# Optimization experiments

Measured on AMD Instinct MI355X. Metric: run time of the kernel, lower is better.

The kernel has to match this reference:

```python
import math
import jax, jax.numpy as jnp
import numpy as np

B = 65536
EMBED = 256
COND = 256
TIME = 128
HID = 256
E = 8
RHID = 128
IN_DIM = EMBED + TIME + COND  # 640


def setup_inputs() -> dict:
    key = jax.random.key(0)
    ks = jax.random.split(key, 20)
    s = 0.02
    inp = {
        "z_t": jax.random.normal(ks[0], (B, EMBED), jnp.float32),
        "t": jax.random.uniform(ks[1], (B, 1), jnp.float32),
        "cond": jax.random.normal(ks[2], (B, COND), jnp.float32),
        # time embedding proj (Linear(time,time) -> SiLU -> Linear(time,time))
        "tW1": jax.random.normal(ks[3], (TIME, TIME), jnp.float32) * s,
        "tb1": jnp.zeros((TIME,), jnp.float32),
        "tW2": jax.random.normal(ks[4], (TIME, TIME), jnp.float32) * s,
        "tb2": jnp.zeros((TIME,), jnp.float32),
        # stacked expert weights [E, in, out]
        "eW1": jax.random.normal(ks[5], (E, IN_DIM, HID), jnp.float32) * s,
        "eb1": jnp.zeros((E, HID), jnp.float32),
        "eW2": jax.random.normal(ks[6], (E, HID, HID), jnp.float32) * s,
        "eb2": jnp.zeros((E, HID), jnp.float32),
        "eW3": jax.random.normal(ks[7], (E, HID, EMBED), jnp.float32) * s,
        "eb3": jnp.zeros((E, EMBED), jnp.float32),
        # router
        "rW1": jax.random.normal(ks[8], (IN_DIM, RHID), jnp.float32) * s,
        "rb1": jnp.zeros((RHID,), jnp.float32),
        "rW2": jax.random.normal(ks[9], (RHID, E), jnp.float32) * s,
        "rb2": jnp.zeros((E,), jnp.float32),
    }
    return inp


def _time_embedding(t, tW1, tb1, tW2, tb2):
    half = TIME // 2  # 64
    scale = -math.log(10000.0) / (half - 1)
    freqs = jnp.exp(jnp.arange(half, dtype=t.dtype) * scale)[None, :]  # [1, half]
    angles = t * freqs  # [B, half]
    emb = jnp.concatenate([jnp.sin(angles), jnp.cos(angles)], axis=-1)  # [B, TIME]
    h = jax.nn.silu(emb @ tW1 + tb1)
    return h @ tW2 + tb2


def reference(z_t, t, cond, tW1, tb1, tW2, tb2, eW1, eb1, eW2, eb2, eW3, eb3, rW1, rb1, rW2, rb2):
    time_emb = _time_embedding(t, tW1, tb1, tW2, tb2)
    x = jnp.concatenate([z_t, time_emb, cond], axis=-1)  # [B, IN_DIM]
    # dense MoE: all experts via batched GEMMs (dropout=0 -> identity)
    h1 = jax.nn.silu(jnp.einsum('bi,eih->beh', x, eW1) + eb1)      # [B,E,HID]
    h2 = jax.nn.silu(jnp.einsum('beh,ehk->bek', h1, eW2) + eb2)    # [B,E,HID]
    expert_out = jnp.einsum('beh,ehd->bed', h2, eW3) + eb3         # [B,E,EMBED]
    # router softmax gate
    rh = jax.nn.silu(x @ rW1 + rb1)
    gate = jax.nn.softmax(rh @ rW2 + rb2, axis=-1)                 # [B,E]
    velocity = jnp.einsum('be,bed->bd', gate, expert_out)          # [B,EMBED]
    return velocity, gate
```

## Files before the change

### kernel.cpp

```cpp
#include <hip/hip_runtime.h>

typedef __attribute__((ext_vector_type(8))) short bf16x8;
typedef __attribute__((ext_vector_type(4))) float f32x4;

#define NB_ROWS 65536
#define D_EMBED 256
#define D_HID   256
#define N_EXP   8
#define D_RHID  128
#define D_IN    640
#define D_H1    2048

#define HSTR 264

static __device__ __forceinline__ ushort f2bf(float f) {
  union { float f; unsigned u; } v; v.f = f;
  unsigned r = v.u + 0x7fffu + ((v.u >> 16) & 1u);
  return (ushort)(r >> 16);
}
static __device__ __forceinline__ float bf2f(ushort h) {
  union { unsigned u; float f; } v; v.u = ((unsigned)h) << 16;
  return v.f;
}
static __device__ __forceinline__ float silu_f(float x) {
  return x / (1.0f + __expf(-x));
}

static __device__ __forceinline__ int kswz(int r, int c) {
  return r * 64 + ((((c) >> 3) ^ (r & 7)) << 3) + ((c) & 7);
}
static __device__ __forceinline__ int gswz(int r, int c) {
  return ((c) & ~63) | (((((c) >> 3) & 7) ^ ((r) & 7)) << 3) | ((c) & 7);
}

__global__ void prep_transpose(const float* __restrict__ src, ushort* __restrict__ dst,
                               int R, int C, int total) {
  int idx = blockIdx.x * 256 + threadIdx.x;
  if (idx >= total) return;
  int rc = R * C;
  int m = idx / rc;
  int rem = idx - m * rc;
  int r = rem / C;
  int c = rem - r * C;
  dst[m * rc + c * R + r] = f2bf(src[idx]);
}
__global__ void prep_transpose_swz(const float* __restrict__ src, ushort* __restrict__ dst,
                                   int R, int C, int total) {
  int idx = blockIdx.x * 256 + threadIdx.x;
  if (idx >= total) return;
  int rc = R * C;
  int m = idx / rc;
  int rem = idx - m * rc;
  int r = rem / C;
  int c = rem - r * C;
  int p = (r & ~63) + (((((r >> 3) & 7) ^ (c & 7)) << 3) | (r & 7));
  dst[m * rc + c * R + p] = f2bf(src[idx]);
}

static __device__ __forceinline__ void glA128_512(const ushort* __restrict__ src, int ld,
                                                  int kt, ushort* dst, int tid, int w) {
  #pragma unroll
  for (int c = 0; c < 2; ++c) {
    int f = c * 8192 + tid * 16;
    int r = f >> 7, ce = (f & 127) >> 1;
    __builtin_amdgcn_global_load_lds(
        (const __attribute__((address_space(1))) void*)(src + (size_t)r * ld + kt + ce),
        (__attribute__((address_space(3))) void*)(dst + ((c * 8192 + w * 1024) >> 1)),
        16, 0, 0);
  }
}
static __device__ __forceinline__ void glB256_512(const ushort* __restrict__ src, int ld,
                                                  int kt, ushort* dst, int tid, int w) {
  #pragma unroll
  for (int c = 0; c < 4; ++c) {
    int f = c * 8192 + tid * 16;
    int r = f >> 7, ce = (f & 127) >> 1;
    __builtin_amdgcn_global_load_lds(
        (const __attribute__((address_space(1))) void*)(src + (size_t)r * ld + kt + ce),
        (__attribute__((address_space(3))) void*)(dst + ((c * 8192 + w * 1024) >> 1)),
        16, 0, 0);
  }
}
static __device__ __forceinline__ void glB128_256(const ushort* __restrict__ src, int ld,
                                                  int kt, ushort* dst, int tid, int w) {
  #pragma unroll
  for (int c = 0; c < 4; ++c) {
    int f = c * 4096 + tid * 16;
    int r = f >> 7, ce = (f & 127) >> 1;
    __builtin_amdgcn_global_load_lds(
        (const __attribute__((address_space(1))) void*)(src + (size_t)r * ld + kt + ce),
        (__attribute__((address_space(3))) void*)(dst + ((c * 4096 + w * 1024) >> 1)),
        16, 0, 0);
  }
}

__global__ __launch_bounds__(512) void time_x_kernel(
    const float* __restrict__ zt, const float* __restrict__ tin,
    const float* __restrict__ cond,
    const ushort* __restrict__ tw1t, const ushort* __restrict__ tw2t,
    const float* __restrict__ tb1, const float* __restrict__ tb2,
    ushort* __restrict__ x) {
  __shared__ __align__(16) ushort sE[128 * 136];
  __shared__ float sFreq[64];
  __shared__ float sB1[128];
  __shared__ float sB2[128];

  const int tid = threadIdx.x;
  const int row0 = blockIdx.x * 128;

  for (int ch = tid; ch < 128 * 64; ch += 512) {
    int r = ch >> 6;
    int c4 = (ch & 63) << 2;
    size_t grow = (size_t)(row0 + r);
    float4 zv = *(const float4*)&zt[grow * 256 + c4];
    ushort4 o; o.x = f2bf(zv.x); o.y = f2bf(zv.y); o.z = f2bf(zv.z); o.w = f2bf(zv.w);
    *(ushort4*)&x[grow * 640 + gswz(r, c4)] = o;
    float4 cv = *(const float4*)&cond[grow * 256 + c4];
    ushort4 o2; o2.x = f2bf(cv.x); o2.y = f2bf(cv.y); o2.z = f2bf(cv.z); o2.w = f2bf(cv.w);
    *(ushort4*)&x[grow * 640 + gswz(r, 384 + c4)] = o2;
  }

  if (tid < 64) sFreq[tid] = __expf((float)tid * (-9.210340371976184f / 63.0f));
  if (tid < 128) { sB1[tid] = tb1[tid]; sB2[tid] = tb2[tid]; }
  __syncthreads();

  {
    int r = tid >> 2;
    int qd = tid & 3;
    float tv = tin[row0 + r];
    int half = qd >> 1;
    int cbase = (qd & 1) * 32;
    ushort* er = &sE[r * 136 + half * 64 + cbase];
    #pragma unroll
    for (int c = 0; c < 32; ++c) {
      float a = tv * sFreq[cbase + c];
      float v = half ? __cosf(a) : __sinf(a);
      er[c] = f2bf(v);
    }
  }
  __syncthreads();

  const int l = tid & 63;
  const int w = tid >> 6;
  const int wm = w >> 1;
  const int wn = w & 1;
  const int lr = l & 15;
  const int lk = (l >> 4) * 8;
  const int q4 = (l >> 4) * 4;

  f32x4 acc[2][4] = {};
  #pragma unroll
  for (int kk = 0; kk < 4; ++kk) {
    int kb = kk * 32 + lk;
    bf16x8 av[2], bv[4];
    #pragma unroll
    for (int mf = 0; mf < 2; ++mf)
      av[mf] = *(const bf16x8*)&sE[(wm * 32 + mf * 16 + lr) * 136 + kb];
    #pragma unroll
    for (int nf = 0; nf < 4; ++nf)
      bv[nf] = *(const bf16x8*)&tw1t[(size_t)(wn * 64 + nf * 16 + lr) * 128 + kb];
    #pragma unroll
    for (int mf = 0; mf < 2; ++mf)
      #pragma unroll
      for (int nf = 0; nf < 4; ++nf)
        acc[mf][nf] = __builtin_amdgcn_mfma_f32_16x16x32_bf16(av[mf], bv[nf], acc[mf][nf], 0, 0, 0);
  }
  __syncthreads();
  #pragma unroll
  for (int mf = 0; mf < 2; ++mf)
    #pragma unroll
    for (int nf = 0; nf < 4; ++nf) {
      int cc = wn * 64 + nf * 16 + lr;
      #pragma unroll
      for (int rg = 0; rg < 4; ++rg) {
        int rr = wm * 32 + mf * 16 + q4 + rg;
        sE[rr * 136 + cc] = f2bf(silu_f(acc[mf][nf][rg] + sB1[cc]));
      }
    }
  __syncthreads();

  f32x4 acc2[2][4] = {};
  #pragma unroll
  for (int kk = 0; kk < 4; ++kk) {
    int kb = kk * 32 + lk;
    bf16x8 av[2], bv[4];
    #pragma unroll
    for (int mf = 0; mf < 2; ++mf)
      av[mf] = *(const bf16x8*)&sE[(wm * 32 + mf * 16 + lr) * 136 + kb];
    #pragma unroll
    for (int nf = 0; nf < 4; ++nf)
      bv[nf] = *(const bf16x8*)&tw2t[(size_t)(wn * 64 + nf * 16 + lr) * 128 + kb];
    #pragma unroll
    for (int mf = 0; mf < 2; ++mf)
      #pragma unroll
      for (int nf = 0; nf < 4; ++nf)
        acc2[mf][nf] = __builtin_amdgcn_mfma_f32_16x16x32_bf16(av[mf], bv[nf], acc2[mf][nf], 0, 0, 0);
  }
  #pragma unroll
  for (int mf = 0; mf < 2; ++mf)
    #pragma unroll
    for (int nf = 0; nf < 4; ++nf) {
      int cc = wn * 64 + nf * 16 + lr;
      #pragma unroll
      for (int rg = 0; rg < 4; ++rg) {
        int rr = wm * 32 + mf * 16 + q4 + rg;
        x[(size_t)(row0 + rr) * 640 + gswz(rr, 256 + cc)] = f2bf(acc2[mf][nf][rg] + sB2[cc]);
      }
    }
}

__global__ __launch_bounds__(256) void router_kernel(
    const ushort* __restrict__ xb, const ushort* __restrict__ rw1t,
    const float* __restrict__ rb1, const float* __restrict__ rW2,
    const float* __restrict__ rb2, float* __restrict__ gatef,
    float* __restrict__ gateo) {
  __shared__ __align__(16) ushort smA[128 * 64];
  __shared__ __align__(16) ushort smB[128 * 64];
  __shared__ __align__(16) ushort rhbuf[128 * 136];
  __shared__ float sW2[128 * 8];

  const int tid = threadIdx.x;
  const int row0 = blockIdx.x * 128;
  for (int i = tid; i < 1024; i += 256) sW2[i] = rW2[i];

  const int l = tid & 63;
  const int w = tid >> 6;
  const int wm = w >> 1, wn = w & 1;
  const int lr = l & 15, lk = (l >> 4) * 8, q4 = (l >> 4) * 4;
  const ushort* xrow = xb + (size_t)row0 * 640;

  f32x4 acc[4][4] = {};
  for (int kt = 0; kt < 640; kt += 64) {
    glB128_256(xrow, 640, kt, smA, tid, w);
    glB128_256(rw1t, 640, kt, smB, tid, w);
    __syncthreads();
    #pragma unroll
    for (int kk = 0; kk < 2; ++kk) {
      int kb = kk * 32 + lk;
      bf16x8 av[4], bv[4];
      #pragma unroll
      for (int mf = 0; mf < 4; ++mf)
        av[mf] = *(const bf16x8*)&smA[kswz(wm * 64 + mf * 16 + lr, kb)];
      #pragma unroll
      for (int nf = 0; nf < 4; ++nf)
        bv[nf] = *(const bf16x8*)&smB[kswz(wn * 64 + nf * 16 + lr, kb)];
      #pragma unroll
      for (int mf = 0; mf < 4; ++mf)
        #pragma unroll
        for (int nf = 0; nf < 4; ++nf)
          acc[mf][nf] = __builtin_amdgcn_mfma_f32_16x16x32_bf16(av[mf], bv[nf], acc[mf][nf], 0, 0, 0);
    }
    __syncthreads();
  }
  #pragma unroll
  for (int nf = 0; nf < 4; ++nf) {
    int cc = wn * 64 + nf * 16 + lr;
    float b1v = rb1[cc];
    #pragma unroll
    for (int mf = 0; mf < 4; ++mf)
      #pragma unroll
      for (int rg = 0; rg < 4; ++rg) {
        int rr = wm * 64 + mf * 16 + q4 + rg;
        rhbuf[rr * 136 + cc] = f2bf(silu_f(acc[mf][nf][rg] + b1v));
      }
  }
  __syncthreads();

  if (tid < 128) {
    float a[8];
    #pragma unroll
    for (int e = 0; e < 8; ++e) a[e] = rb2[e];
    #pragma unroll
    for (int i8 = 0; i8 < 16; ++i8) {
      bf16x8 hv = *(const bf16x8*)&rhbuf[tid * 136 + i8 * 8];
      #pragma unroll
      for (int j = 0; j < 8; ++j) {
        float h = bf2f((ushort)hv[j]);
        const float* wrow = &sW2[(i8 * 8 + j) * 8];
        #pragma unroll
        for (int e = 0; e < 8; ++e) a[e] += h * wrow[e];
      }
    }
    float mx = a[0];
    #pragma unroll
    for (int e = 1; e < 8; ++e) mx = fmaxf(mx, a[e]);
    float s = 0.f, ex[8];
    #pragma unroll
    for (int e = 0; e < 8; ++e) { ex[e] = __expf(a[e] - mx); s += ex[e]; }
    float inv = 1.f / s;
    size_t b = (size_t)(row0 + tid);
    #pragma unroll
    for (int e = 0; e < 8; ++e) {
      float g = ex[e] * inv;
      gatef[b * 8 + e] = g;
      gateo[b * 8 + e] = g;
    }
  }
}

__global__ __launch_bounds__(512) void moe_h1_kernel(
    const ushort* __restrict__ xb, const ushort* __restrict__ w1t,
    const float* __restrict__ eb1, ushort* __restrict__ hg, int row_base) {
  __shared__ __align__(16) ushort smA[128 * 64];
  __shared__ __align__(16) ushort smB[256 * 64];

  const int tid = threadIdx.x;
  int nwg = gridDim.x;
  int flat = blockIdx.x;
  int sid = (flat & 7) * (nwg >> 3) + (flat >> 3);
  const int rb = sid >> 3;
  const int e  = sid & 7;
  const int lrow0 = rb * 128;

  const int l = tid & 63;
  const int w = tid >> 6;
  const int wm = w >> 2, wn = w & 3;
  const int lr = l & 15, lk = (l >> 4) * 8, q4 = (l >> 4) * 4;

  const ushort* xrow = xb + (size_t)(row_base + lrow0) * 640;
  const ushort* W1 = w1t + (size_t)e * (256 * 640);

  f32x4 acc[4][4] = {};
  for (int kt = 0; kt < 640; kt += 64) {
    glA128_512(xrow, 640, kt, smA, tid, w);
    glB256_512(W1, 640, kt, smB, tid, w);
    __syncthreads();
    #pragma unroll
    for (int kk = 0; kk < 2; ++kk) {
      int kb = kk * 32 + lk;
      bf16x8 av[4], bv[4];
      #pragma unroll
      for (int mf = 0; mf < 4; ++mf)
        av[mf] = *(const bf16x8*)&smA[kswz(wm * 64 + mf * 16 + lr, kb)];
      #pragma unroll
      for (int nf = 0; nf < 4; ++nf)
        bv[nf] = *(const bf16x8*)&smB[kswz(wn * 64 + nf * 16 + lr, kb)];
      #pragma unroll
      for (int mf = 0; mf < 4; ++mf)
        #pragma unroll
        for (int nf = 0; nf < 4; ++nf)
          acc[mf][nf] = __builtin_amdgcn_mfma_f32_16x16x32_bf16(av[mf], bv[nf], acc[mf][nf], 0, 0, 0);
    }
    __syncthreads();
  }
  #pragma unroll
  for (int nf = 0; nf < 4; ++nf) {
    int cc = wn * 64 + nf * 16 + lr;
    float b1v = eb1[e * 256 + cc];
    #pragma unroll
    for (int mf = 0; mf < 4; ++mf)
      #pragma unroll
      for (int rg = 0; rg < 4; ++rg) {
        int rr = wm * 64 + mf * 16 + q4 + rg;
        hg[(size_t)(lrow0 + rr) * D_H1 + e * 256 + gswz(rr, cc)] =
            f2bf(silu_f(acc[mf][nf][rg] + b1v));
      }
  }
}

__global__ __launch_bounds__(512) void moe_h2_kernel(
    ushort* __restrict__ hg, const ushort* __restrict__ w2t,
    const float* __restrict__ eb2, const float* __restrict__ gatef, int row_base) {
  __shared__ __align__(16) ushort smA[128 * 64];
  __shared__ __align__(16) ushort smB[256 * 64];
  __shared__ float sGate[128];

  const int tid = threadIdx.x;
  int nwg = gridDim.x;
  int flat = blockIdx.x;
  int sid = (flat & 7) * (nwg >> 3) + (flat >> 3);
  const int rb = sid >> 3;
  const int e  = sid & 7;
  const int lrow0 = rb * 128;

  const int l = tid & 63;
  const int w = tid >> 6;
  const int wm = w >> 2, wn = w & 3;
  const int lr = l & 15, lk = (l >> 4) * 8, q4 = (l >> 4) * 4;

  if (tid < 128) sGate[tid] = gatef[(size_t)(row_base + lrow0 + tid) * 8 + e];

  ushort* hrow = hg + (size_t)lrow0 * D_H1 + e * 256;
  const ushort* W2 = w2t + (size_t)e * (256 * 256);

  f32x4 acc[4][4] = {};
  for (int kt = 0; kt < 256; kt += 64) {
    glA128_512(hrow, D_H1, kt, smA, tid, w);
    glB256_512(W2, 256, kt, smB, tid, w);
    __syncthreads();
    #pragma unroll
    for (int kk = 0; kk < 2; ++kk) {
      int kb = kk * 32 + lk;
      bf16x8 av[4], bv[4];
      #pragma unroll
      for (int mf = 0; mf < 4; ++mf)
        av[mf] = *(const bf16x8*)&smA[kswz(wm * 64 + mf * 16 + lr, kb)];
      #pragma unroll
      for (int nf = 0; nf < 4; ++nf)
        bv[nf] = *(const bf16x8*)&smB[kswz(wn * 64 + nf * 16 + lr, kb)];
      #pragma unroll
      for (int mf = 0; mf < 4; ++mf)
        #pragma unroll
        for (int nf = 0; nf < 4; ++nf)
          acc[mf][nf] = __builtin_amdgcn_mfma_f32_16x16x32_bf16(av[mf], bv[nf], acc[mf][nf], 0, 0, 0);
    }
    __syncthreads();
  }
  #pragma unroll
  for (int nf = 0; nf < 4; ++nf) {
    int cc = wn * 64 + nf * 16 + lr;
    float b2v = eb2[e * 256 + cc];
    #pragma unroll
    for (int mf = 0; mf < 4; ++mf)
      #pragma unroll
      for (int rg = 0; rg < 4; ++rg) {
        int rr = wm * 64 + mf * 16 + q4 + rg;
        hrow[(size_t)rr * D_H1 + gswz(rr, cc)] =
            f2bf(silu_f(acc[mf][nf][rg] + b2v) * sGate[rr]);
      }
  }
}

__global__ __launch_bounds__(512) void moe_vel_kernel(
    const ushort* __restrict__ hg, const ushort* __restrict__ w3t,
    const float* __restrict__ eb3, const float* __restrict__ gatef,
    float* __restrict__ velout, int row_base) {
  __shared__ __align__(16) ushort smA[128 * 64];
  __shared__ __align__(16) ushort smB[256 * 64];
  __shared__ float sGate[128 * 8];

  const int tid = threadIdx.x;
  int nwg = gridDim.x;
  int flat = blockIdx.x;
  int sid = (flat & 7) * (nwg >> 3) + (flat >> 3);
  const int lrow0 = sid * 128;

  const int l = tid & 63;
  const int w = tid >> 6;
  const int wm = w >> 2, wn = w & 3;
  const int lr = l & 15, lk = (l >> 4) * 8, q4 = (l >> 4) * 4;

  for (int i = tid; i < 1024; i += 512) sGate[i] = gatef[(size_t)(row_base + lrow0) * 8 + i];

  const ushort* hrow = hg + (size_t)lrow0 * D_H1;
  f32x4 vacc[4][4] = {};
  __syncthreads();

  for (int kt = 0; kt < 2048; kt += 64) {
    const int e = kt >> 8;
    glA128_512(hrow, D_H1, kt, smA, tid, w);
    glB256_512(w3t + (size_t)e * (256 * 256), 256, kt & 255, smB, tid, w);
    __syncthreads();
    #pragma unroll
    for (int kk = 0; kk < 2; ++kk) {
      int kb = kk * 32 + lk;
      bf16x8 av[4], bv[4];
      #pragma unroll
      for (int mf = 0; mf < 4; ++mf)
        av[mf] = *(const bf16x8*)&smA[kswz(wm * 64 + mf * 16 + lr, kb)];
      #pragma unroll
      for (int nf = 0; nf < 4; ++nf)
        bv[nf] = *(const bf16x8*)&smB[kswz(wn * 64 + nf * 16 + lr, kb)];
      #pragma unroll
      for (int mf = 0; mf < 4; ++mf)
        #pragma unroll
        for (int nf = 0; nf < 4; ++nf)
          vacc[mf][nf] = __builtin_amdgcn_mfma_f32_16x16x32_bf16(av[mf], bv[nf], vacc[mf][nf], 0, 0, 0);
    }
    __syncthreads();
  }

  float* eL = (float*)smB;
  for (int i = tid; i < 2048; i += 512) eL[i] = eb3[i];
  __syncthreads();
  #pragma unroll
  for (int mf = 0; mf < 4; ++mf)
    #pragma unroll
    for (int rg = 0; rg < 4; ++rg) {
      int rr = wm * 64 + mf * 16 + q4 + rg;
      const float* gp = &sGate[rr * 8];
      #pragma unroll
      for (int nf = 0; nf < 4; ++nf) {
        int cc = wn * 64 + nf * 16 + lr;
        float bsum = 0.f;
        #pragma unroll
        for (int ee = 0; ee < 8; ++ee) bsum += gp[ee] * eL[ee * 256 + cc];
        velout[(size_t)(row_base + lrow0 + rr) * D_EMBED + cc] = vacc[mf][nf][rg] + bsum;
      }
    }
}

__global__ __launch_bounds__(512) void moe_fused_kernel(
    const ushort* __restrict__ xb, const ushort* __restrict__ w1t,
    const ushort* __restrict__ w2t, const ushort* __restrict__ w3t,
    const float* __restrict__ eb1, const float* __restrict__ eb2,
    const float* __restrict__ eb3, const float* __restrict__ gatef,
    float* __restrict__ velout) {
  __shared__ __align__(16) ushort smA[128 * 64];
  __shared__ __align__(16) ushort smB[256 * 64];
  __shared__ __align__(16) ushort hbuf[128 * HSTR];
  __shared__ float sGate[128 * 8];
  __shared__ float sEb3[8 * 256];

  const int tid = threadIdx.x;
  const int row0 = blockIdx.x * 128;
  const int l = tid & 63;
  const int w = tid >> 6;
  const int wm = w >> 2, wn = w & 3;
  const int lr = l & 15, lk = (l >> 4) * 8, q4 = (l >> 4) * 4;

  for (int i = tid; i < 1024; i += 512) sGate[i] = gatef[(size_t)row0 * 8 + i];
  for (int i = tid; i < 2048; i += 512) sEb3[i] = eb3[i];

  const ushort* xrow = xb + (size_t)row0 * 640;
  f32x4 vacc[4][4] = {};
  __syncthreads();

  for (int e = 0; e < 8; ++e) {
    const ushort* W1 = w1t + (size_t)e * (256 * 640);
    const ushort* W2 = w2t + (size_t)e * (256 * 256);
    const ushort* W3 = w3t + (size_t)e * (256 * 256);

    f32x4 acc[4][4] = {};
    for (int kt = 0; kt < 640; kt += 64) {
      glA128_512(xrow, 640, kt, smA, tid, w);
      glB256_512(W1, 640, kt, smB, tid, w);
      __syncthreads();
      #pragma unroll
      for (int kk = 0; kk < 2; ++kk) {
        int kb = kk * 32 + lk;
        bf16x8 av[4], bv[4];
        #pragma unroll
        for (int mf = 0; mf < 4; ++mf)
          av[mf] = *(const bf16x8*)&smA[kswz(wm * 64 + mf * 16 + lr, kb)];
        #pragma unroll
        for (int nf = 0; nf < 4; ++nf)
          bv[nf] = *(const bf16x8*)&smB[kswz(wn * 64 + nf * 16 + lr, kb)];
        #pragma unroll
        for (int mf = 0; mf < 4; ++mf)
          #pragma unroll
          for (int nf = 0; nf < 4; ++nf)
            acc[mf][nf] = __builtin_amdgcn_mfma_f32_16x16x32_bf16(av[mf], bv[nf], acc[mf][nf], 0, 0, 0);
      }
      __syncthreads();
    }
    #pragma unroll
    for (int nf = 0; nf < 4; ++nf) {
      int cc = wn * 64 + nf * 16 + lr;
      float b1v = eb1[e * 256 + cc];
      #pragma unroll
      for (int mf = 0; mf < 4; ++mf)
        #pragma unroll
        for (int rg = 0; rg < 4; ++rg) {
          int rr = wm * 64 + mf * 16 + q4 + rg;
          hbuf[rr * HSTR + cc] = f2bf(silu_f(acc[mf][nf][rg] + b1v));
        }
    }
    __syncthreads();

    #pragma unroll
    for (int mf = 0; mf < 4; ++mf)
      #pragma unroll
      for (int nf = 0; nf < 4; ++nf)
        acc[mf][nf] = (f32x4){0.f, 0.f, 0.f, 0.f};
    for (int kt = 0; kt < 256; kt += 64) {
      glB256_512(W2, 256, kt, smB, tid, w);
      __syncthreads();
      #pragma unroll
      for (int kk = 0; kk < 2; ++kk) {
        int kbl = kk * 32 + lk;
        int kbh = kt + kbl;
        bf16x8 av[4], bv[4];
        #pragma unroll
        for (int mf = 0; mf < 4; ++mf)
          av[mf] = *(const bf16x8*)&hbuf[(wm * 64 + mf * 16 + lr) * HSTR + kbh];
        #pragma unroll
        for (int nf = 0; nf < 4; ++nf)
          bv[nf] = *(const bf16x8*)&smB[kswz(wn * 64 + nf * 16 + lr, kbl)];
        #pragma unroll
        for (int mf = 0; mf < 4; ++mf)
          #pragma unroll
          for (int nf = 0; nf < 4; ++nf)
            acc[mf][nf] = __builtin_amdgcn_mfma_f32_16x16x32_bf16(av[mf], bv[nf], acc[mf][nf], 0, 0, 0);
      }
      __syncthreads();
    }
    #pragma unroll
    for (int nf = 0; nf < 4; ++nf) {
      int cc = wn * 64 + nf * 16 + lr;
      float b2v = eb2[e * 256 + cc];
      #pragma unroll
      for (int mf = 0; mf < 4; ++mf)
        #pragma unroll
        for (int rg = 0; rg < 4; ++rg) {
          int rr = wm * 64 + mf * 16 + q4 + rg;
          float gv = sGate[rr * 8 + e];
          hbuf[rr * HSTR + cc] = f2bf(silu_f(acc[mf][nf][rg] + b2v) * gv);
        }
    }
    __syncthreads();

    for (int kt = 0; kt < 256; kt += 64) {
      glB256_512(W3, 256, kt, smB, tid, w);
      __syncthreads();
      #pragma unroll
      for (int kk = 0; kk < 2; ++kk) {
        int kbl = kk * 32 + lk;
        int kbh = kt + kbl;
        bf16x8 av[4], bv[4];
        #pragma unroll
        for (int mf = 0; mf < 4; ++mf)
          av[mf] = *(const bf16x8*)&hbuf[(wm * 64 + mf * 16 + lr) * HSTR + kbh];
        #pragma unroll
        for (int nf = 0; nf < 4; ++nf)
          bv[nf] = *(const bf16x8*)&smB[kswz(wn * 64 + nf * 16 + lr, kbl)];
        #pragma unroll
        for (int mf = 0; mf < 4; ++mf)
          #pragma unroll
          for (int nf = 0; nf < 4; ++nf)
            vacc[mf][nf] = __builtin_amdgcn_mfma_f32_16x16x32_bf16(av[mf], bv[nf], vacc[mf][nf], 0, 0, 0);
      }
      __syncthreads();
    }
  }

  #pragma unroll
  for (int mf = 0; mf < 4; ++mf)
    #pragma unroll
    for (int rg = 0; rg < 4; ++rg) {
      int rr = wm * 64 + mf * 16 + q4 + rg;
      const float* gp = &sGate[rr * 8];
      #pragma unroll
      for (int nf = 0; nf < 4; ++nf) {
        int cc = wn * 64 + nf * 16 + lr;
        float bsum = 0.f;
        #pragma unroll
        for (int ee = 0; ee < 8; ++ee) bsum += gp[ee] * sEb3[ee * 256 + cc];
        velout[(size_t)(row0 + rr) * D_EMBED + cc] = vacc[mf][nf][rg] + bsum;
      }
    }
}

extern "C" void kernel_launch(void* const* d_in, const int* in_sizes, int n_in,
                              void* d_out, int out_size, void* d_ws, size_t ws_size,
                              hipStream_t stream) {
  const float* zt   = (const float*)d_in[0];
  const float* tin  = (const float*)d_in[1];
  const float* cond = (const float*)d_in[2];
  const float* tW1  = (const float*)d_in[3];
  const float* tb1  = (const float*)d_in[4];
  const float* tW2  = (const float*)d_in[5];
  const float* tb2  = (const float*)d_in[6];
  const float* eW1  = (const float*)d_in[7];
  const float* eb1  = (const float*)d_in[8];
  const float* eW2  = (const float*)d_in[9];
  const float* eb2  = (const float*)d_in[10];
  const float* eW3  = (const float*)d_in[11];
  const float* eb3  = (const float*)d_in[12];
  const float* rW1  = (const float*)d_in[13];
  const float* rb1  = (const float*)d_in[14];
  const float* rW2  = (const float*)d_in[15];
  const float* rb2  = (const float*)d_in[16];

  char* wp = (char*)d_ws;
  ushort* xb    = (ushort*)wp; wp += (size_t)NB_ROWS * D_IN * 2;
  float*  gatef = (float*)wp;  wp += (size_t)NB_ROWS * 8 * 4;
  ushort* w1t   = (ushort*)wp; wp += (size_t)N_EXP * D_HID * D_IN * 2;
  ushort* w2t   = (ushort*)wp; wp += (size_t)N_EXP * D_HID * D_HID * 2;
  ushort* w3t   = (ushort*)wp; wp += (size_t)N_EXP * D_HID * D_EMBED * 2;
  ushort* rw1t  = (ushort*)wp; wp += (size_t)D_RHID * D_IN * 2;
  ushort* tw1t  = (ushort*)wp; wp += (size_t)128 * 128 * 2;
  ushort* tw2t  = (ushort*)wp; wp += (size_t)128 * 128 * 2;
  ushort* hg    = (ushort*)wp;
  size_t base = (size_t)(wp - (char*)d_ws);

  int CH = 0;
  for (int cand = NB_ROWS; cand >= 8192; cand >>= 1) {
    if (base + (size_t)cand * D_H1 * 2 <= ws_size) { CH = cand; break; }
  }

  float* velout  = (float*)d_out;
  float* gateout = velout + (size_t)NB_ROWS * D_EMBED;

  {
    int tot;
    tot = 128 * 128;
    prep_transpose<<<(tot + 255) / 256, 256, 0, stream>>>(tW1, tw1t, 128, 128, tot);
    prep_transpose<<<(tot + 255) / 256, 256, 0, stream>>>(tW2, tw2t, 128, 128, tot);
    tot = D_IN * D_RHID;
    prep_transpose_swz<<<(tot + 255) / 256, 256, 0, stream>>>(rW1, rw1t, D_IN, D_RHID, tot);
    tot = N_EXP * D_IN * D_HID;
    prep_transpose_swz<<<(tot + 255) / 256, 256, 0, stream>>>(eW1, w1t, D_IN, D_HID, tot);
    tot = N_EXP * D_HID * D_HID;
    prep_transpose_swz<<<(tot + 255) / 256, 256, 0, stream>>>(eW2, w2t, D_HID, D_HID, tot);
    tot = N_EXP * D_HID * D_EMBED;
    prep_transpose_swz<<<(tot + 255) / 256, 256, 0, stream>>>(eW3, w3t, D_HID, D_EMBED, tot);
  }

  time_x_kernel<<<512, 512, 0, stream>>>(zt, tin, cond, tw1t, tw2t, tb1, tb2, xb);
  router_kernel<<<512, 256, 0, stream>>>(xb, rw1t, rb1, rW2, rb2, gatef, gateout);

  if (CH > 0) {
    for (int r0 = 0; r0 < NB_ROWS; r0 += CH) {
      moe_h1_kernel<<<(CH / 128) * 8, 512, 0, stream>>>(xb, w1t, eb1, hg, r0);
      moe_h2_kernel<<<(CH / 128) * 8, 512, 0, stream>>>(hg, w2t, eb2, gatef, r0);
      moe_vel_kernel<<<CH / 128, 512, 0, stream>>>(hg, w3t, eb3, gatef, velout, r0);
    }
  } else {
    moe_fused_kernel<<<512, 512, 0, stream>>>(xb, w1t, w2t, w3t,
                                              eb1, eb2, eb3, gatef, velout);
  }
}
```

Baseline: 656.6 us.

## Precompute load/LDS addresses in MoE GEMMs and halve vel-kernel row tile

Hoists global-load source pointers and swizzled LDS read offsets out of the K loops in the h1, h2 and velocity kernels, so each iteration only advances pointers instead of recomputing addresses. The velocity kernel's row tile drops from 128 to 64 rows and the grid doubles, to get more workgroups across CUs. The fused path inlines the same loads. The smaller vel tile lowers reuse of each W3 tile and raises total weight traffic, and the hoisted addresses add register pressure.

```diff
diff --git a/kernel.cpp b/kernel.cpp
--- a/kernel.cpp
+++ b/kernel.cpp
@@ -31,6 +31,12 @@
 }
 static __device__ __forceinline__ int gswz(int r, int c) {
   return ((c) & ~63) | (((((c) >> 3) & 7) ^ ((r) & 7)) << 3) | ((c) & 7);
+}
+
+static __device__ __forceinline__ void gl16(const ushort* src, ushort* dst) {
+  __builtin_amdgcn_global_load_lds(
+      (const __attribute__((address_space(1))) void*)src,
+      (__attribute__((address_space(3))) void*)dst, 16, 0, 0);
 }
 
 __global__ void prep_transpose(const float* __restrict__ src, ushort* __restrict__ dst,
@@ -57,40 +63,13 @@
   dst[m * rc + c * R + p] = f2bf(src[idx]);
 }
 
-static __device__ __forceinline__ void glA128_512(const ushort* __restrict__ src, int ld,
-                                                  int kt, ushort* dst, int tid, int w) {
-  #pragma unroll
-  for (int c = 0; c < 2; ++c) {
-    int f = c * 8192 + tid * 16;
-    int r = f >> 7, ce = (f & 127) >> 1;
-    __builtin_amdgcn_global_load_lds(
-        (const __attribute__((address_space(1))) void*)(src + (size_t)r * ld + kt + ce),
-        (__attribute__((address_space(3))) void*)(dst + ((c * 8192 + w * 1024) >> 1)),
-        16, 0, 0);
-  }
-}
-static __device__ __forceinline__ void glB256_512(const ushort* __restrict__ src, int ld,
-                                                  int kt, ushort* dst, int tid, int w) {
-  #pragma unroll
-  for (int c = 0; c < 4; ++c) {
-    int f = c * 8192 + tid * 16;
-    int r = f >> 7, ce = (f & 127) >> 1;
-    __builtin_amdgcn_global_load_lds(
-        (const __attribute__((address_space(1))) void*)(src + (size_t)r * ld + kt + ce),
-        (__attribute__((address_space(3))) void*)(dst + ((c * 8192 + w * 1024) >> 1)),
-        16, 0, 0);
-  }
-}
 static __device__ __forceinline__ void glB128_256(const ushort* __restrict__ src, int ld,
                                                   int kt, ushort* dst, int tid, int w) {
   #pragma unroll
   for (int c = 0; c < 4; ++c) {
     int f = c * 4096 + tid * 16;
     int r = f >> 7, ce = (f & 127) >> 1;
-    __builtin_amdgcn_global_load_lds(
-        (const __attribute__((address_space(1))) void*)(src + (size_t)r * ld + kt + ce),
-        (__attribute__((address_space(3))) void*)(dst + ((c * 4096 + w * 1024) >> 1)),
-        16, 0, 0);
+    gl16(src + (size_t)r * ld + kt + ce, dst + ((c * 4096 + w * 1024) >> 1));
   }
 }
 
@@ -320,21 +299,45 @@
   const ushort* xrow = xb + (size_t)(row_base + lrow0) * 640;
   const ushort* W1 = w1t + (size_t)e * (256 * 640);
 
+  const ushort* aS[2]; ushort* aD[2];
+  #pragma unroll
+  for (int c = 0; c < 2; ++c) {
+    int f = c * 8192 + tid * 16;
+    int r = f >> 7, ce = (f & 127) >> 1;
+    aS[c] = xrow + (size_t)r * 640 + ce;
+    aD[c] = smA + ((c * 8192 + w * 1024) >> 1);
+  }
+  const ushort* bS[4]; ushort* bD[4];
+  #pragma unroll
+  for (int c = 0; c < 4; ++c) {
+    int f = c * 8192 + tid * 16;
+    int r = f >> 7, ce = (f & 127) >> 1;
+    bS[c] = W1 + (size_t)r * 640 + ce;
+    bD[c] = smB + ((c * 8192 + w * 1024) >> 1);
+  }
+  int oA[2][4], oB[2][4];
+  #pragma unroll
+  for (int kk = 0; kk < 2; ++kk) {
+    #pragma unroll
+    for (int mf = 0; mf < 4; ++mf) oA[kk][mf] = kswz(wm * 64 + mf * 16 + lr, kk * 32 + lk);
+    #pragma unroll
+    for (int nf = 0; nf < 4; ++nf) oB[kk][nf] = kswz(wn * 64 + nf * 16 + lr, kk * 32 + lk);
+  }
+
   f32x4 acc[4][4] = {};
   for (int kt = 0; kt < 640; kt += 64) {
-    glA128_512(xrow, 640, kt, smA, tid, w);
-    glB256_512(W1, 640, kt, smB, tid, w);
+    #pragma unroll
+    for (int c = 0; c < 2; ++c) { gl16(aS[c], aD[c]); aS[c] += 64; }
+    #pragma unroll
+    for (int c = 0; c < 4; ++c) { gl16(bS[c], bD[c]); bS[c] += 64; }
     __syncthreads();
     #pragma unroll
     for (int kk = 0; kk < 2; ++kk) {
-      int kb = kk * 32 + lk;
       bf16x8 av[4], bv[4];
       #pragma unroll
-      for (int mf = 0; mf < 4; ++mf)
-        av[mf] = *(const bf16x8*)&smA[kswz(wm * 64 + mf * 16 + lr, kb)];
-      #pragma unroll
-      for (int nf = 0; nf < 4; ++nf)
-        bv[nf] = *(const bf16x8*)&smB[kswz(wn * 64 + nf * 16 + lr, kb)];
+      for (int mf = 0; mf < 4; ++mf) av[mf] = *(const bf16x8*)&smA[oA[kk][mf]];
+      #pragma unroll
+      for (int nf = 0; nf < 4; ++nf) bv[nf] = *(const bf16x8*)&smB[oB[kk][nf]];
       #pragma unroll
       for (int mf = 0; mf < 4; ++mf)
         #pragma unroll
@@ -383,21 +386,45 @@
   ushort* hrow = hg + (size_t)lrow0 * D_H1 + e * 256;
   const ushort* W2 = w2t + (size_t)e * (256 * 256);
 
+  const ushort* aS[2]; ushort* aD[2];
+  #pragma unroll
+  for (int c = 0; c < 2; ++c) {
+    int f = c * 8192 + tid * 16;
+    int r = f >> 7, ce = (f & 127) >> 1;
+    aS[c] = hrow + (size_t)r * D_H1 + ce;
+    aD[c] = smA + ((c * 8192 + w * 1024) >> 1);
+  }
+  const ushort* bS[4]; ushort* bD[4];
+  #pragma unroll
+  for (int c = 0; c < 4; ++c) {
+    int f = c * 8192 + tid * 16;
+    int r = f >> 7, ce = (f & 127) >> 1;
+    bS[c] = W2 + (size_t)r * 256 + ce;
+    bD[c] = smB + ((c * 8192 + w * 1024) >> 1);
+  }
+  int oA[2][4], oB[2][4];
+  #pragma unroll
+  for (int kk = 0; kk < 2; ++kk) {
+    #pragma unroll
+    for (int mf = 0; mf < 4; ++mf) oA[kk][mf] = kswz(wm * 64 + mf * 16 + lr, kk * 32 + lk);
+    #pragma unroll
+    for (int nf = 0; nf < 4; ++nf) oB[kk][nf] = kswz(wn * 64 + nf * 16 + lr, kk * 32 + lk);
+  }
+
   f32x4 acc[4][4] = {};
   for (int kt = 0; kt < 256; kt += 64) {
-    glA128_512(hrow, D_H1, kt, smA, tid, w);
-    glB256_512(W2, 256, kt, smB, tid, w);
+    #pragma unroll
+    for (int c = 0; c < 2; ++c) { gl16(aS[c], aD[c]); aS[c] += 64; }
+    #pragma unroll
+    for (int c = 0; c < 4; ++c) { gl16(bS[c], bD[c]); bS[c] += 64; }
     __syncthreads();
     #pragma unroll
     for (int kk = 0; kk < 2; ++kk) {
-      int kb = kk * 32 + lk;
       bf16x8 av[4], bv[4];
       #pragma unroll
-      for (int mf = 0; mf < 4; ++mf)
-        av[mf] = *(const bf16x8*)&smA[kswz(wm * 64 + mf * 16 + lr, kb)];
-      #pragma unroll
-      for (int nf = 0; nf < 4; ++nf)
-        bv[nf] = *(const bf16x8*)&smB[kswz(wn * 64 + nf * 16 + lr, kb)];
+      for (int mf = 0; mf < 4; ++mf) av[mf] = *(const bf16x8*)&smA[oA[kk][mf]];
+      #pragma unroll
+      for (int nf = 0; nf < 4; ++nf) bv[nf] = *(const bf16x8*)&smB[oB[kk][nf]];
       #pragma unroll
       for (int mf = 0; mf < 4; ++mf)
         #pragma unroll
@@ -425,59 +452,87 @@
     const ushort* __restrict__ hg, const ushort* __restrict__ w3t,
     const float* __restrict__ eb3, const float* __restrict__ gatef,
     float* __restrict__ velout, int row_base) {
-  __shared__ __align__(16) ushort smA[128 * 64];
+  __shared__ __align__(16) ushort smA[64 * 64];
   __shared__ __align__(16) ushort smB[256 * 64];
-  __shared__ float sGate[128 * 8];
+  __shared__ float sGate[64 * 8];
 
   const int tid = threadIdx.x;
   int nwg = gridDim.x;
   int flat = blockIdx.x;
   int sid = (flat & 7) * (nwg >> 3) + (flat >> 3);
-  const int lrow0 = sid * 128;
+  const int lrow0 = sid * 64;
 
   const int l = tid & 63;
   const int w = tid >> 6;
   const int wm = w >> 2, wn = w & 3;
   const int lr = l & 15, lk = (l >> 4) * 8, q4 = (l >> 4) * 4;
 
-  for (int i = tid; i < 1024; i += 512) sGate[i] = gatef[(size_t)(row_base + lrow0) * 8 + i];
+  if (tid < 512) sGate[tid] = gatef[(size_t)(row_base + lrow0) * 8 + tid];
 
   const ushort* hrow = hg + (size_t)lrow0 * D_H1;
-  f32x4 vacc[4][4] = {};
+
+  const ushort* aS; ushort* aD;
+  {
+    int f = tid * 16;
+    int r = f >> 7, ce = (f & 127) >> 1;
+    aS = hrow + (size_t)r * D_H1 + ce;
+    aD = smA + ((tid * 16) >> 1);
+  }
+  int bR[4], bC[4]; ushort* bD[4];
+  #pragma unroll
+  for (int c = 0; c < 4; ++c) {
+    int f = c * 8192 + tid * 16;
+    bR[c] = f >> 7; bC[c] = (f & 127) >> 1;
+    bD[c] = smB + ((c * 8192 + w * 1024) >> 1);
+  }
+  int oA[2][2], oB[2][4];
+  #pragma unroll
+  for (int kk = 0; kk < 2; ++kk) {
+    #pragma unroll
+    for (int mf = 0; mf < 2; ++mf) oA[kk][mf] = kswz(wm * 32 + mf * 16 + lr, kk * 32 + lk);
+    #pragma unroll
+    for (int nf = 0; nf < 4; ++nf) oB[kk][nf] = kswz(wn * 64 + nf * 16 + lr, kk * 32 + lk);
+  }
+
+  f32x4 vacc[2][4] = {};
   __syncthreads();
 
-  for (int kt = 0; kt < 2048; kt += 64) {
-    const int e = kt >> 8;
-    glA128_512(hrow, D_H1, kt, smA, tid, w);
-    glB256_512(w3t + (size_t)e * (256 * 256), 256, kt & 255, smB, tid, w);
-    __syncthreads();
-    #pragma unroll
-    for (int kk = 0; kk < 2; ++kk) {
-      int kb = kk * 32 + lk;
-      bf16x8 av[4], bv[4];
-      #pragma unroll
-      for (int mf = 0; mf < 4; ++mf)
-        av[mf] = *(const bf16x8*)&smA[kswz(wm * 64 + mf * 16 + lr, kb)];
-      #pragma unroll
-      for (int nf = 0; nf < 4; ++nf)
-        bv[nf] = *(const bf16x8*)&smB[kswz(wn * 64 + nf * 16 + lr, kb)];
-      #pragma unroll
-      for (int mf = 0; mf < 4; ++mf)
-        #pragma unroll
-        for (int nf = 0; nf < 4; ++nf)
-          vacc[mf][nf] = __builtin_amdgcn_mfma_f32_16x16x32_bf16(av[mf], bv[nf], vacc[mf][nf], 0, 0, 0);
-    }
-    __syncthreads();
+  for (int e = 0; e < 8; ++e) {
+    const ushort* bS[4];
+    const ushort* W3 = w3t + (size_t)e * (256 * 256);
+    #pragma unroll
+    for (int c = 0; c < 4; ++c) bS[c] = W3 + (size_t)bR[c] * 256 + bC[c];
+    #pragma unroll
+    for (int t4 = 0; t4 < 4; ++t4) {
+      gl16(aS, aD); aS += 64;
+      #pragma unroll
+      for (int c = 0; c < 4; ++c) { gl16(bS[c], bD[c]); bS[c] += 64; }
+      __syncthreads();
+      #pragma unroll
+      for (int kk = 0; kk < 2; ++kk) {
+        bf16x8 av[2], bv[4];
+        #pragma unroll
+        for (int mf = 0; mf < 2; ++mf) av[mf] = *(const bf16x8*)&smA[oA[kk][mf]];
+        #pragma unroll
+        for (int nf = 0; nf < 4; ++nf) bv[nf] = *(const bf16x8*)&smB[oB[kk][nf]];
+        #pragma unroll
+        for (int mf = 0; mf < 2; ++mf)
+          #pragma unroll
+          for (int nf = 0; nf < 4; ++nf)
+            vacc[mf][nf] = __builtin_amdgcn_mfma_f32_16x16x32_bf16(av[mf], bv[nf], vacc[mf][nf], 0, 0, 0);
+      }
+      __syncthreads();
+    }
   }
 
   float* eL = (float*)smB;
   for (int i = tid; i < 2048; i += 512) eL[i] = eb3[i];
   __syncthreads();
   #pragma unroll
-  for (int mf = 0; mf < 4; ++mf)
+  for (int mf = 0; mf < 2; ++mf)
     #pragma unroll
     for (int rg = 0; rg < 4; ++rg) {
-      int rr = wm * 64 + mf * 16 + q4 + rg;
+      int rr = wm * 32 + mf * 16 + q4 + rg;
       const float* gp = &sGate[rr * 8];
       #pragma unroll
       for (int nf = 0; nf < 4; ++nf) {
@@ -523,8 +578,18 @@
 
     f32x4 acc[4][4] = {};
     for (int kt = 0; kt < 640; kt += 64) {
-      glA128_512(xrow, 640, kt, smA, tid, w);
-      glB256_512(W1, 640, kt, smB, tid, w);
+      #pragma unroll
+      for (int c = 0; c < 2; ++c) {
+        int f = c * 8192 + tid * 16;
+        int r = f >> 7, ce = (f & 127) >> 1;
+        gl16(xrow + (size_t)r * 640 + kt + ce, smA + ((c * 8192 + w * 1024) >> 1));
+      }
+      #pragma unroll
+      for (int c = 0; c < 4; ++c) {
+        int f = c * 8192 + tid * 16;
+        int r = f >> 7, ce = (f & 127) >> 1;
+        gl16(W1 + (size_t)r * 640 + kt + ce, smB + ((c * 8192 + w * 1024) >> 1));
+      }
       __syncthreads();
       #pragma unroll
       for (int kk = 0; kk < 2; ++kk) {
@@ -564,7 +629,12 @@
       for (int nf = 0; nf < 4; ++nf)
         acc[mf][nf] = (f32x4){0.f, 0.f, 0.f, 0.f};
     for (int kt = 0; kt < 256; kt += 64) {
-      glB256_512(W2, 256, kt, smB, tid, w);
+      #pragma unroll
+      for (int c = 0; c < 4; ++c) {
+        int f = c * 8192 + tid * 16;
+        int r = f >> 7, ce = (f & 127) >> 1;
+        gl16(W2 + (size_t)r * 256 + kt + ce, smB + ((c * 8192 + w * 1024) >> 1));
+      }
       __syncthreads();
       #pragma unroll
       for (int kk = 0; kk < 2; ++kk) {
@@ -601,7 +671,12 @@
     __syncthreads();
 
     for (int kt = 0; kt < 256; kt += 64) {
-      glB256_512(W3, 256, kt, smB, tid, w);
+      #pragma unroll
+      for (int c = 0; c < 4; ++c) {
+        int f = c * 8192 + tid * 16;
+        int r = f >> 7, ce = (f & 127) >> 1;
+        gl16(W3 + (size_t)r * 256 + kt + ce, smB + ((c * 8192 + w * 1024) >> 1));
+      }
       __syncthreads();
       #pragma unroll
       for (int kk = 0; kk < 2; ++kk) {
@@ -704,7 +779,7 @@
     for (int r0 = 0; r0 < NB_ROWS; r0 += CH) {
       moe_h1_kernel<<<(CH / 128) * 8, 512, 0, stream>>>(xb, w1t, eb1, hg, r0);
       moe_h2_kernel<<<(CH / 128) * 8, 512, 0, stream>>>(hg, w2t, eb2, gatef, r0);
-      moe_vel_kernel<<<CH / 128, 512, 0, stream>>>(hg, w3t, eb3, gatef, velout, r0);
+      moe_vel_kernel<<<CH / 64, 512, 0, stream>>>(hg, w3t, eb3, gatef, velout, r0);
     }
   } else {
     moe_fused_kernel<<<512, 512, 0, stream>>>(xb, w1t, w2t, w3t,
```

Result: faster. 634.5 us (-3.4%).
